# Performance work log

Hardware: AMD Instinct MI355X
Metric: run time of the kernel (lower is better)

The kernel has to match this reference:

```python
import jax, jax.numpy as jnp
import numpy as np

HIDDEN = 2048
N_HEADS = 32
N_KV_HEADS = 8
HEAD_DIM = HIDDEN // N_HEADS  # 64
N_REP = N_HEADS // N_KV_HEADS  # 4
ROPE_THETA = 10000.0


def setup_inputs() -> dict:
    key = jax.random.key(0)
    ks = jax.random.split(key, 5)
    b, s = 2, 2048
    x = jax.random.normal(ks[0], (b, s, HIDDEN), dtype=jnp.float32)
    position_ids = jnp.arange(b * s, dtype=jnp.int32).reshape(b, s)
    sc = 1.0 / np.sqrt(HIDDEN)
    Wq = jax.random.normal(ks[1], (HIDDEN, HIDDEN), dtype=jnp.float32) * sc
    Wk = jax.random.normal(ks[2], (HIDDEN, N_KV_HEADS * HEAD_DIM), dtype=jnp.float32) * sc
    Wv = jax.random.normal(ks[3], (HIDDEN, N_KV_HEADS * HEAD_DIM), dtype=jnp.float32) * sc
    Wo = jax.random.normal(ks[4], (HIDDEN, HIDDEN), dtype=jnp.float32) * sc
    return {"input_ids": x, "Wq": Wq, "Wk": Wk, "Wv": Wv, "Wo": Wo,
            "position_ids": position_ids}


def _rope_cos_sin(position_ids, dtype):
    # inv_freq: [head_dim/2]
    inv_freq = 1.0 / (ROPE_THETA ** (jnp.arange(0, HEAD_DIM, 2, dtype=jnp.float32) / HEAD_DIM))
    freqs = position_ids.astype(jnp.float32)[..., None] * inv_freq  # [b, s, d/2]
    emb = jnp.concatenate([freqs, freqs], axis=-1)  # [b, s, d]
    return emb.astype(dtype), None  # placeholder, replaced below


def _rotate_half(x):
    x1, x2 = jnp.split(x, 2, axis=-1)
    return jnp.concatenate([-x2, x1], axis=-1)


def reference(input_ids, Wq, Wk, Wv, Wo, position_ids):
    b, s, _ = input_ids.shape
    q = (input_ids @ Wq).reshape(b, s, N_HEADS, HEAD_DIM).transpose(0, 2, 1, 3)      # [b,H,s,d]
    k = (input_ids @ Wk).reshape(b, s, N_KV_HEADS, HEAD_DIM).transpose(0, 2, 1, 3)   # [b,Hkv,s,d]
    v = (input_ids @ Wv).reshape(b, s, N_KV_HEADS, HEAD_DIM).transpose(0, 2, 1, 3)

    # RoPE
    inv_freq = 1.0 / (ROPE_THETA ** (jnp.arange(0, HEAD_DIM, 2, dtype=jnp.float32) / HEAD_DIM))
    freqs = position_ids.astype(jnp.float32)[..., None] * inv_freq  # [b,s,d/2]
    emb = jnp.concatenate([freqs, freqs], axis=-1)                   # [b,s,d]
    cos = jnp.cos(emb).astype(input_ids.dtype)[:, None, :, :]        # [b,1,s,d]
    sin = jnp.sin(emb).astype(input_ids.dtype)[:, None, :, :]
    q = q * cos + _rotate_half(q) * sin
    k = k * cos + _rotate_half(k) * sin

    # repeat_kv: [b,Hkv,s,d] -> [b,H,s,d]
    k = jnp.repeat(k, N_REP, axis=1)
    v = jnp.repeat(v, N_REP, axis=1)

    # causal SDPA
    scale = 1.0 / np.sqrt(HEAD_DIM)
    scores = jnp.einsum('bhqd,bhkd->bhqk', q, k) * scale
    causal = jnp.tril(jnp.ones((s, s), dtype=bool))
    scores = jnp.where(causal, scores, jnp.finfo(scores.dtype).min)
    attn = jax.nn.softmax(scores, axis=-1)
    out = jnp.einsum('bhqk,bhkd->bhqd', attn, v)                     # [b,H,s,d]
    out = out.transpose(0, 2, 1, 3).reshape(b, s, HIDDEN)
    return out @ Wo
```

## Files before the change

kernel.cpp:

```cpp
#include <hip/hip_runtime.h>
#include <hip/hip_bf16.h>

#define HIDDEN 2048
#define NHEADS 32
#define NKVH   8
#define HD     64
#define BATCH  2
#define SEQ    2048
#define ROWS   (BATCH * SEQ)
#define NQKV   3072
#define KCOL   2048
#define VCOL   2560

typedef __bf16 bf16x8 __attribute__((ext_vector_type(8)));
typedef __bf16 bf16x4 __attribute__((ext_vector_type(4)));
typedef float  f32x4  __attribute__((ext_vector_type(4)));
typedef short  s16x4  __attribute__((ext_vector_type(4)));
typedef short  s16x8  __attribute__((ext_vector_type(8)));

__device__ __forceinline__ void gl2lds16(const void* g, void* l) {
  __builtin_amdgcn_global_load_lds(
      (const __attribute__((address_space(1))) void*)g,
      (__attribute__((address_space(3))) void*)l, 16, 0, 0);
}

__device__ __forceinline__ short f2bs(float f) {
  __bf16 h = (__bf16)f;
  return __builtin_bit_cast(short, h);
}

__device__ __forceinline__ float fexp2(float x) {
#if __has_builtin(__builtin_amdgcn_exp2f)
  return __builtin_amdgcn_exp2f(x);
#else
  return exp2f(x);
#endif
}

__device__ __forceinline__ f32x4 mfma16(s16x4 a, s16x4 b, f32x4 c) {
#if __has_builtin(__builtin_amdgcn_mfma_f32_16x16x16bf16_1k)
  return __builtin_amdgcn_mfma_f32_16x16x16bf16_1k(a, b, c, 0, 0, 0);
#else
  s16x8 a8 = __builtin_shufflevector(a, (s16x4){0,0,0,0}, 0,1,2,3,4,5,6,7);
  s16x8 b8 = __builtin_shufflevector(b, (s16x4){0,0,0,0}, 0,1,2,3,4,5,6,7);
  a8[4]=0;a8[5]=0;a8[6]=0;a8[7]=0; b8[4]=0;b8[5]=0;b8[6]=0;b8[7]=0;
  return __builtin_amdgcn_mfma_f32_16x16x32_bf16(
      __builtin_bit_cast(bf16x8, a8), __builtin_bit_cast(bf16x8, b8), c, 0, 0, 0);
#endif
}

__global__ void prep(const float* __restrict__ Wq, const float* __restrict__ Wk,
                     const float* __restrict__ Wv, const float* __restrict__ Wo,
                     const float* __restrict__ x,
                     __bf16* __restrict__ dstW, __bf16* __restrict__ Xb) {
  int bid = blockIdx.x, t = threadIdx.x;
  if (bid < 2560) {
    __shared__ __bf16 tl[32][132];
    int k0 = (bid & 15) * 128;
    int n0 = (bid >> 4) * 32;
    const float* src;
    int N, c0;
    if (n0 < 2048)      { src = Wq; N = 2048; c0 = n0; }
    else if (n0 < 2560) { src = Wk; N = 512;  c0 = n0 - 2048; }
    else if (n0 < 3072) { src = Wv; N = 512;  c0 = n0 - 2560; }
    else                { src = Wo; N = 2048; c0 = n0 - 3072; }
    int rr = t >> 3;
    int cc = (t & 7) * 4;
#pragma unroll
    for (int pass = 0; pass < 4; ++pass) {
      int k = pass * 32 + rr;
      float4 v = *(const float4*)(src + (size_t)(k0 + k) * N + c0 + cc);
      tl[cc + 0][k] = (__bf16)v.x;
      tl[cc + 1][k] = (__bf16)v.y;
      tl[cc + 2][k] = (__bf16)v.z;
      tl[cc + 3][k] = (__bf16)v.w;
    }
    __syncthreads();
    int n = t >> 4;
    int ch = t & 15;
#pragma unroll
    for (int it = 0; it < 2; ++it) {
      int nn = n + it * 16;
      s16x4 lo = *(const s16x4*)(&tl[nn][ch * 8]);
      s16x4 hi = *(const s16x4*)(&tl[nn][ch * 8 + 4]);
      s16x8 o = __builtin_shufflevector(lo, hi, 0, 1, 2, 3, 4, 5, 6, 7);
      *(s16x8*)(dstW + (size_t)(n0 + nn) * HIDDEN + k0 + ch * 8) = o;
    }
  } else {
    size_t i = (size_t)(bid - 2560) * 256 + t;
    const float4* s = (const float4*)(x + i * 16);
    float4 a = s[0], b = s[1], c = s[2], d = s[3];
    bf16x8 o0, o1;
    o0[0] = (__bf16)a.x; o0[1] = (__bf16)a.y; o0[2] = (__bf16)a.z; o0[3] = (__bf16)a.w;
    o0[4] = (__bf16)b.x; o0[5] = (__bf16)b.y; o0[6] = (__bf16)b.z; o0[7] = (__bf16)b.w;
    o1[0] = (__bf16)c.x; o1[1] = (__bf16)c.y; o1[2] = (__bf16)c.z; o1[3] = (__bf16)c.w;
    o1[4] = (__bf16)d.x; o1[5] = (__bf16)d.y; o1[6] = (__bf16)d.z; o1[7] = (__bf16)d.w;
    *(bf16x8*)(Xb + i * 16)     = o0;
    *(bf16x8*)(Xb + i * 16 + 8) = o1;
  }
}

template <typename OutT, bool ROPE>
__launch_bounds__(256, 2)
__global__ void gemm_bt(const __bf16* __restrict__ A, const __bf16* __restrict__ Bt,
                        OutT* __restrict__ C, int M, int N, int K,
                        const int* __restrict__ pos_ids, __bf16* __restrict__ Vt) {
  __shared__ __bf16 As[2][128 * 32];
  __shared__ __bf16 Bs[2][128 * 32];
  int id = blockIdx.x;
  int bm = (id & 7) * 4 + ((id >> 3) & 3);
  int bn = id >> 5;
  int t = threadIdx.x;
  int wave = t >> 6, lane = t & 63, l16 = lane & 15, quad = lane >> 4;
  int wm = (wave >> 1) * 64, wn = (wave & 1) * 64;

  f32x4 acc[4][4] = {};

  int arow = t >> 2;
  int ac   = (t & 3) * 8;
  const __bf16* Ag = A  + (size_t)(bm * 128 + arow) * K + ac;
  const __bf16* Bg = Bt + (size_t)(bn * 128 + arow) * K + ac;
  int woff = wave * 512;

  for (int k0 = 0; k0 < K; k0 += 64) {
    __syncthreads();
    gl2lds16(Ag + k0,                      &As[0][woff]);
    gl2lds16(Ag + (size_t)64 * K + k0,      &As[0][2048 + woff]);
    gl2lds16(Ag + k0 + 32,                 &As[1][woff]);
    gl2lds16(Ag + (size_t)64 * K + k0 + 32, &As[1][2048 + woff]);
    gl2lds16(Bg + k0,                      &Bs[0][woff]);
    gl2lds16(Bg + (size_t)64 * K + k0,      &Bs[0][2048 + woff]);
    gl2lds16(Bg + k0 + 32,                 &Bs[1][woff]);
    gl2lds16(Bg + (size_t)64 * K + k0 + 32, &Bs[1][2048 + woff]);
    __syncthreads();

#pragma unroll
    for (int ks = 0; ks < 2; ++ks) {
      bf16x8 af[4], bfr[4];
#pragma unroll
      for (int i = 0; i < 4; ++i) {
        af[i]  = *(const bf16x8*)(&As[ks][(wm + i * 16 + l16) * 32 + quad * 8]);
        bfr[i] = *(const bf16x8*)(&Bs[ks][(wn + i * 16 + l16) * 32 + quad * 8]);
      }
#pragma unroll
      for (int i = 0; i < 4; ++i)
#pragma unroll
        for (int j = 0; j < 4; ++j)
          acc[i][j] = __builtin_amdgcn_mfma_f32_16x16x32_bf16(af[i], bfr[j], acc[i][j], 0, 0, 0);
    }
  }

  if (ROPE) {
    int headidx = bn * 2 + (wn >> 6);
    if (headidx >= 40) {
#pragma unroll
      for (int i = 0; i < 4; ++i) {
        int srow = bm * 128 + wm + i * 16 + quad * 4;
        int b = srow >> 11, s = srow & 2047;
#pragma unroll
        for (int j = 0; j < 4; ++j) {
          int vcol = bn * 128 + wn + j * 16 + l16 - VCOL;
          int hk = vcol >> 6, d = vcol & 63;
          bf16x4 w;
#pragma unroll
          for (int r = 0; r < 4; ++r) w[r] = (__bf16)acc[i][j][r];
          *(bf16x4*)(Vt + ((size_t)(b * NKVH + hk) * HD + d) * SEQ + s) = w;
        }
      }
      return;
    }
    float invrev0 = __expf(-(float)l16 * 0.28782313662425574f) * 0.15915494309189535f;
    float invrev1 = __expf(-(float)(l16 + 16) * 0.28782313662425574f) * 0.15915494309189535f;
#pragma unroll
    for (int i = 0; i < 4; ++i)
#pragma unroll
      for (int r = 0; r < 4; ++r) {
        int gr = bm * 128 + wm + i * 16 + quad * 4 + r;
        float pos = (float)pos_ids[gr];
        float rv0 = pos * invrev0; rv0 -= floorf(rv0);
        float rv1 = pos * invrev1; rv1 -= floorf(rv1);
        float a0 = rv0 * 6.283185307179586f, a1 = rv1 * 6.283185307179586f;
        float s0 = __sinf(a0), c0 = __cosf(a0);
        float s1 = __sinf(a1), c1 = __cosf(a1);
        float x0 = acc[i][0][r], x2 = acc[i][2][r];
        acc[i][0][r] = x0 * c0 - x2 * s0;
        acc[i][2][r] = x2 * c0 + x0 * s0;
        float x1 = acc[i][1][r], x3 = acc[i][3][r];
        acc[i][1][r] = x1 * c1 - x3 * s1;
        acc[i][3][r] = x3 * c1 + x1 * s1;
      }
  }

#pragma unroll
  for (int i = 0; i < 4; ++i)
#pragma unroll
    for (int j = 0; j < 4; ++j)
#pragma unroll
      for (int r = 0; r < 4; ++r)
        C[(size_t)(bm * 128 + wm + i * 16 + quad * 4 + r) * N +
          (bn * 128 + wn + j * 16 + l16)] = (OutT)acc[i][j][r];
}

__launch_bounds__(256, 4)
__global__ void flash_attn(const __bf16* __restrict__ QKV, const __bf16* __restrict__ Vt,
                           __bf16* __restrict__ O) {
  int wgid = blockIdx.x + 64 * (blockIdx.y + 8 * (int)blockIdx.z);
  int xcd  = wgid & 7;
  int j    = wgid >> 3;
  int G    = j >> 6;
  int gid  = xcd * 2 + G;
  int b    = gid >> 3;
  int hk   = gid & 7;
  int r    = j & 63;
  int b0   = r & 1, b5 = (r >> 5) & 1;
  int h    = hk * 4 + b0 + 2 * b5;
  int M0   = (r >> 1) & 15;
  int M    = (b0 ^ b5) ? (15 - M0) : M0;
  int NT   = 2 * M + 2;

  int t = threadIdx.x;
  int wave = t >> 6, lane = t & 63, l16 = lane & 15, quad = lane >> 4;

  __shared__ __bf16 Ks[2][2][64 * 32];
  __shared__ __bf16 Vs[2][4096];

  const __bf16* Kbase = QKV + (size_t)(b * SEQ) * NQKV + KCOL + hk * HD;
  const __bf16* VtB   = Vt + (size_t)(b * NKVH + hk) * HD * SEQ;

  int kr  = wave * 16 + (lane >> 2);
  int kcs = ((lane & 3) ^ ((lane >> 3) & 3)) * 8;
  int rq  = (quad ^ ((l16 >> 1) & 3)) * 8;

  int vd   = kr;
  int vsc  = (lane & 3) * 16;
  int vs4w = (lane & 3) * 4;
  int vcw4 = (vd ^ (4 * (lane & 3))) * 4;

  const s16x4 vones = { (short)0x3F80, (short)0x3F80, (short)0x3F80, (short)0x3F80 };

  bf16x8 qfrag[2][2];
#pragma unroll
  for (int qi = 0; qi < 2; ++qi) {
    const __bf16* qp = QKV + (size_t)(b * SEQ + M * 128 + qi * 64 + wave * 16 + l16) * NQKV
                     + h * HD + quad * 8;
    bf16x8 q0 = *(const bf16x8*)qp;
    bf16x8 q1 = *(const bf16x8*)(qp + 32);
#pragma unroll
    for (int e = 0; e < 8; ++e) {
      qfrag[qi][0][e] = (__bf16)((float)q0[e] * 0.18033688011112042f);
      qfrag[qi][1][e] = (__bf16)((float)q1[e] * 0.18033688011112042f);
    }
  }

  f32x4 lacc[2] = { {0.f,0.f,0.f,0.f}, {0.f,0.f,0.f,0.f} };
  f32x4 oacc[2][4];
#pragma unroll
  for (int qi = 0; qi < 2; ++qi)
#pragma unroll
    for (int dt = 0; dt < 4; ++dt) oacc[qi][dt] = (f32x4){0.f, 0.f, 0.f, 0.f};

  {
    const __bf16* kp = Kbase + (size_t)kr * NQKV + kcs;
    gl2lds16(kp,      &Ks[0][0][wave * 512]);
    gl2lds16(kp + 32, &Ks[0][1][wave * 512]);
    const __bf16* vp = VtB + (size_t)vd * SEQ + vsc;
    s16x8 v0 = __builtin_bit_cast(s16x8, *(const bf16x8*)vp);
    s16x8 v1 = __builtin_bit_cast(s16x8, *(const bf16x8*)(vp + 8));
    *(s16x4*)(&Vs[0][(vs4w + 0) * 256 + vcw4]) = __builtin_shufflevector(v0, v0, 0, 1, 2, 3);
    *(s16x4*)(&Vs[0][(vs4w + 1) * 256 + vcw4]) = __builtin_shufflevector(v0, v0, 4, 5, 6, 7);
    *(s16x4*)(&Vs[0][(vs4w + 2) * 256 + vcw4]) = __builtin_shufflevector(v1, v1, 0, 1, 2, 3);
    *(s16x4*)(&Vs[0][(vs4w + 3) * 256 + vcw4]) = __builtin_shufflevector(v1, v1, 4, 5, 6, 7);
  }

  for (int kt = 0; kt < NT; ++kt) {
    int buf = kt & 1;
    __syncthreads();

    bool pre = (kt < NT - 1);
    s16x8 pv0, pv1;
    if (pre) {
      const __bf16* kp = Kbase + (size_t)((kt + 1) * 64 + kr) * NQKV + kcs;
      gl2lds16(kp,      &Ks[buf ^ 1][0][wave * 512]);
      gl2lds16(kp + 32, &Ks[buf ^ 1][1][wave * 512]);
      const __bf16* vp = VtB + (size_t)vd * SEQ + (kt + 1) * 64 + vsc;
      pv0 = __builtin_bit_cast(s16x8, *(const bf16x8*)vp);
      pv1 = __builtin_bit_cast(s16x8, *(const bf16x8*)(vp + 8));
    }

    f32x4 s0[4], s1[4];
#pragma unroll
    for (int nt = 0; nt < 4; ++nt) {
      s0[nt] = (f32x4){0.f, 0.f, 0.f, 0.f};
      s1[nt] = (f32x4){0.f, 0.f, 0.f, 0.f};
    }
#pragma unroll
    for (int ks = 0; ks < 2; ++ks) {
      bf16x8 kf[4];
#pragma unroll
      for (int nt = 0; nt < 4; ++nt)
        kf[nt] = *(const bf16x8*)(&Ks[buf][ks][(nt * 16 + l16) * 32 + rq]);
#pragma unroll
      for (int nt = 0; nt < 4; ++nt)
        s1[nt] = __builtin_amdgcn_mfma_f32_16x16x32_bf16(kf[nt], qfrag[1][ks], s1[nt], 0, 0, 0);
      if (pre) {
#pragma unroll
        for (int nt = 0; nt < 4; ++nt)
          s0[nt] = __builtin_amdgcn_mfma_f32_16x16x32_bf16(kf[nt], qfrag[0][ks], s0[nt], 0, 0, 0);
      }
    }

    s16x4 af0[4], af1[4];
    {
      int qg = wave * 16 + l16;
      if (kt == NT - 1) {
#pragma unroll
        for (int nt = 0; nt < 4; ++nt)
#pragma unroll
          for (int rr = 0; rr < 4; ++rr) {
            int kg = nt * 16 + quad * 4 + rr;
            af1[nt][rr] = f2bs(fexp2((kg > qg) ? -1e30f : s1[nt][rr]));
          }
      } else {
#pragma unroll
        for (int nt = 0; nt < 4; ++nt)
#pragma unroll
          for (int rr = 0; rr < 4; ++rr)
            af1[nt][rr] = f2bs(fexp2(s1[nt][rr]));
      }
      if (pre) {
        if (kt == NT - 2) {
#pragma unroll
          for (int nt = 0; nt < 4; ++nt)
#pragma unroll
            for (int rr = 0; rr < 4; ++rr) {
              int kg = nt * 16 + quad * 4 + rr;
              af0[nt][rr] = f2bs(fexp2((kg > qg) ? -1e30f : s0[nt][rr]));
            }
        } else {
#pragma unroll
          for (int nt = 0; nt < 4; ++nt)
#pragma unroll
            for (int rr = 0; rr < 4; ++rr)
              af0[nt][rr] = f2bs(fexp2(s0[nt][rr]));
        }
      }
    }

#pragma unroll
    for (int nt = 0; nt < 4; ++nt) {
      s16x4 vf[4];
#pragma unroll
      for (int dt = 0; dt < 4; ++dt)
        vf[dt] = *(const s16x4*)(&Vs[buf][(nt * 4 + quad) * 256 +
                                          (((dt * 16 + l16) ^ (nt * 4)) * 4)]);
#pragma unroll
      for (int dt = 0; dt < 4; ++dt)
        oacc[1][dt] = mfma16(af1[nt], vf[dt], oacc[1][dt]);
      lacc[1] = mfma16(af1[nt], vones, lacc[1]);
      if (pre) {
#pragma unroll
        for (int dt = 0; dt < 4; ++dt)
          oacc[0][dt] = mfma16(af0[nt], vf[dt], oacc[0][dt]);
        lacc[0] = mfma16(af0[nt], vones, lacc[0]);
      }
    }

    if (pre) {
      *(s16x4*)(&Vs[buf ^ 1][(vs4w + 0) * 256 + vcw4]) = __builtin_shufflevector(pv0, pv0, 0, 1, 2, 3);
      *(s16x4*)(&Vs[buf ^ 1][(vs4w + 1) * 256 + vcw4]) = __builtin_shufflevector(pv0, pv0, 4, 5, 6, 7);
      *(s16x4*)(&Vs[buf ^ 1][(vs4w + 2) * 256 + vcw4]) = __builtin_shufflevector(pv1, pv1, 0, 1, 2, 3);
      *(s16x4*)(&Vs[buf ^ 1][(vs4w + 3) * 256 + vcw4]) = __builtin_shufflevector(pv1, pv1, 4, 5, 6, 7);
    }
  }

#pragma unroll
  for (int qi = 0; qi < 2; ++qi) {
#pragma unroll
    for (int rr = 0; rr < 4; ++rr) {
      float inv = 1.0f / lacc[qi][rr];
#pragma unroll
      for (int dt = 0; dt < 4; ++dt) {
        float o = oacc[qi][dt][rr] * inv;
        O[(size_t)(b * SEQ + M * 128 + qi * 64 + wave * 16 + quad * 4 + rr) * HIDDEN +
          h * HD + dt * 16 + l16] = (__bf16)o;
      }
    }
  }
}

extern "C" void kernel_launch(void* const* d_in, const int* in_sizes, int n_in,
                              void* d_out, int out_size, void* d_ws, size_t ws_size,
                              hipStream_t stream) {
  const float* x  = (const float*)d_in[0];
  const float* Wq = (const float*)d_in[1];
  const float* Wk = (const float*)d_in[2];
  const float* Wv = (const float*)d_in[3];
  const float* Wo = (const float*)d_in[4];
  const int* pos  = (const int*)d_in[5];

  __bf16* Wqkvt = (__bf16*)d_ws;
  __bf16* Wot   = Wqkvt + (size_t)NQKV * HIDDEN;
  __bf16* Xb    = Wot + (size_t)HIDDEN * HIDDEN;
  __bf16* QKV   = Xb + (size_t)ROWS * HIDDEN;
  __bf16* Oat   = QKV + (size_t)ROWS * NQKV;
  __bf16* Vt    = Xb;

  prep<<<dim3(4608), 256, 0, stream>>>(Wq, Wk, Wv, Wo, x, Wqkvt, Xb);

  gemm_bt<__bf16, true><<<dim3(768), 256, 0, stream>>>(
      Xb, Wqkvt, QKV, ROWS, NQKV, HIDDEN, pos, Vt);

  flash_attn<<<dim3(64, NKVH, BATCH), 256, 0, stream>>>(QKV, Vt, Oat);

  gemm_bt<float, false><<<dim3(512), 256, 0, stream>>>(
      Oat, Wot, (float*)d_out, ROWS, HIDDEN, HIDDEN, nullptr, nullptr);
}
```

Measured before the change: 266.3 us.

## Replace QKV projection GEMM with 256x256-tile swizzled kernel and separate Vt buffer

Adds a dedicated QKV GEMM kernel that uses 256x256 output tiles, 512 threads, a 64-wide K step and XOR-swizzled LDS staging, with the RoPE and V-transpose epilogue carried over. Each block maps to an XCD-aware (bm, bn) pair. The goal is more reuse per LDS load and fewer bank conflicts than the generic 128x128 kernel. The trade-off is that only 192 blocks are launched, each using about 128KB of LDS and heavy accumulator registers, so some CUs may sit idle. Vt now goes to a dedicated workspace region when space allows, instead of aliasing the X buffer that the GEMM is still reading.

```diff
diff --git a/kernel.cpp b/kernel.cpp
--- a/kernel.cpp
+++ b/kernel.cpp
@@ -100,11 +100,123 @@
   }
 }
 
-template <typename OutT, bool ROPE>
+__launch_bounds__(512, 2)
+__global__ void gemm_qkv256(const __bf16* __restrict__ A, const __bf16* __restrict__ Bt,
+                            __bf16* __restrict__ C,
+                            const int* __restrict__ pos_ids, __bf16* __restrict__ Vt) {
+  __shared__ __bf16 As[2][16384];
+  __shared__ __bf16 Bs[2][16384];
+
+  int id = blockIdx.x;
+  int xcd = id & 7, j = id >> 3;
+  int bm = xcd * 2 + (j >= 12 ? 1 : 0);
+  int bn = (j >= 12) ? (j - 12) : j;
+
+  int t = threadIdx.x;
+  int wave = t >> 6, lane = t & 63, l16 = lane & 15, quad = lane >> 4;
+  int wml = (wave & 1) * 128;
+  int wnl = (wave >> 1) * 64;
+
+  int srow = wave * 8 + (lane >> 3);
+  int csrc = ((lane & 7) ^ (lane >> 3)) * 8;
+  const __bf16* Ag = A  + (size_t)(bm * 256 + srow) * HIDDEN + csrc;
+  const __bf16* Bg = Bt + (size_t)(bn * 256 + srow) * HIDDEN + csrc;
+
+  f32x4 acc[8][4] = {};
+
+#pragma unroll
+  for (int jj = 0; jj < 4; ++jj) {
+    gl2lds16(Ag + (size_t)jj * 64 * HIDDEN, &As[0][(jj * 64 + wave * 8) * 64]);
+    gl2lds16(Bg + (size_t)jj * 64 * HIDDEN, &Bs[0][(jj * 64 + wave * 8) * 64]);
+  }
+
+  for (int kt = 0; kt < 32; ++kt) {
+    int s = kt & 1;
+    __syncthreads();
+    if (kt < 31) {
+      const __bf16* Agk = Ag + (kt + 1) * 64;
+      const __bf16* Bgk = Bg + (kt + 1) * 64;
+#pragma unroll
+      for (int jj = 0; jj < 4; ++jj) {
+        gl2lds16(Agk + (size_t)jj * 64 * HIDDEN, &As[s ^ 1][(jj * 64 + wave * 8) * 64]);
+        gl2lds16(Bgk + (size_t)jj * 64 * HIDDEN, &Bs[s ^ 1][(jj * 64 + wave * 8) * 64]);
+      }
+    }
+#pragma unroll
+    for (int ks = 0; ks < 2; ++ks) {
+      int ch8 = (((ks * 4 + quad) ^ (l16 & 7))) * 8;
+      bf16x8 bfr[4];
+#pragma unroll
+      for (int n = 0; n < 4; ++n)
+        bfr[n] = *(const bf16x8*)(&Bs[s][(wnl + n * 16 + l16) * 64 + ch8]);
+#pragma unroll
+      for (int mh = 0; mh < 2; ++mh) {
+        bf16x8 af[4];
+#pragma unroll
+        for (int m = 0; m < 4; ++m)
+          af[m] = *(const bf16x8*)(&As[s][(wml + mh * 64 + m * 16 + l16) * 64 + ch8]);
+#pragma unroll
+        for (int m = 0; m < 4; ++m)
+#pragma unroll
+          for (int n = 0; n < 4; ++n)
+            acc[mh * 4 + m][n] =
+                __builtin_amdgcn_mfma_f32_16x16x32_bf16(af[m], bfr[n], acc[mh * 4 + m][n], 0, 0, 0);
+      }
+    }
+  }
+
+  int headidx = bn * 4 + (wave >> 1);
+  if (headidx >= 40) {
+    int hk = headidx - 40;
+#pragma unroll
+    for (int m = 0; m < 8; ++m) {
+      int gr0 = bm * 256 + wml + m * 16 + quad * 4;
+      int b = gr0 >> 11, sq = gr0 & 2047;
+#pragma unroll
+      for (int n = 0; n < 4; ++n) {
+        int d = n * 16 + l16;
+        bf16x4 w;
+#pragma unroll
+        for (int r = 0; r < 4; ++r) w[r] = (__bf16)acc[m][n][r];
+        *(bf16x4*)(Vt + ((size_t)(b * NKVH + hk) * HD + d) * SEQ + sq) = w;
+      }
+    }
+    return;
+  }
+  float invrev0 = __expf(-(float)l16 * 0.28782313662425574f) * 0.15915494309189535f;
+  float invrev1 = __expf(-(float)(l16 + 16) * 0.28782313662425574f) * 0.15915494309189535f;
+#pragma unroll
+  for (int m = 0; m < 8; ++m)
+#pragma unroll
+    for (int r = 0; r < 4; ++r) {
+      int gr = bm * 256 + wml + m * 16 + quad * 4 + r;
+      float pos = (float)pos_ids[gr];
+      float rv0 = pos * invrev0; rv0 -= floorf(rv0);
+      float rv1 = pos * invrev1; rv1 -= floorf(rv1);
+      float a0 = rv0 * 6.283185307179586f, a1 = rv1 * 6.283185307179586f;
+      float s0 = __sinf(a0), c0 = __cosf(a0);
+      float s1 = __sinf(a1), c1 = __cosf(a1);
+      float x0 = acc[m][0][r], x2 = acc[m][2][r];
+      acc[m][0][r] = x0 * c0 - x2 * s0;
+      acc[m][2][r] = x2 * c0 + x0 * s0;
+      float x1 = acc[m][1][r], x3 = acc[m][3][r];
+      acc[m][1][r] = x1 * c1 - x3 * s1;
+      acc[m][3][r] = x3 * c1 + x1 * s1;
+    }
+#pragma unroll
+  for (int m = 0; m < 8; ++m)
+#pragma unroll
+    for (int n = 0; n < 4; ++n)
+#pragma unroll
+      for (int r = 0; r < 4; ++r)
+        C[(size_t)(bm * 256 + wml + m * 16 + quad * 4 + r) * NQKV +
+          (bn * 256 + wnl + n * 16 + l16)] = (__bf16)acc[m][n][r];
+}
+
+template <typename OutT>
 __launch_bounds__(256, 2)
 __global__ void gemm_bt(const __bf16* __restrict__ A, const __bf16* __restrict__ Bt,
-                        OutT* __restrict__ C, int M, int N, int K,
-                        const int* __restrict__ pos_ids, __bf16* __restrict__ Vt) {
+                        OutT* __restrict__ C, int M, int N, int K) {
   __shared__ __bf16 As[2][128 * 32];
   __shared__ __bf16 Bs[2][128 * 32];
   int id = blockIdx.x;
@@ -148,47 +260,6 @@
         for (int j = 0; j < 4; ++j)
           acc[i][j] = __builtin_amdgcn_mfma_f32_16x16x32_bf16(af[i], bfr[j], acc[i][j], 0, 0, 0);
     }
-  }
-
-  if (ROPE) {
-    int headidx = bn * 2 + (wn >> 6);
-    if (headidx >= 40) {
-#pragma unroll
-      for (int i = 0; i < 4; ++i) {
-        int srow = bm * 128 + wm + i * 16 + quad * 4;
-        int b = srow >> 11, s = srow & 2047;
-#pragma unroll
-        for (int j = 0; j < 4; ++j) {
-          int vcol = bn * 128 + wn + j * 16 + l16 - VCOL;
-          int hk = vcol >> 6, d = vcol & 63;
-          bf16x4 w;
-#pragma unroll
-          for (int r = 0; r < 4; ++r) w[r] = (__bf16)acc[i][j][r];
-          *(bf16x4*)(Vt + ((size_t)(b * NKVH + hk) * HD + d) * SEQ + s) = w;
-        }
-      }
-      return;
-    }
-    float invrev0 = __expf(-(float)l16 * 0.28782313662425574f) * 0.15915494309189535f;
-    float invrev1 = __expf(-(float)(l16 + 16) * 0.28782313662425574f) * 0.15915494309189535f;
-#pragma unroll
-    for (int i = 0; i < 4; ++i)
-#pragma unroll
-      for (int r = 0; r < 4; ++r) {
-        int gr = bm * 128 + wm + i * 16 + quad * 4 + r;
-        float pos = (float)pos_ids[gr];
-        float rv0 = pos * invrev0; rv0 -= floorf(rv0);
-        float rv1 = pos * invrev1; rv1 -= floorf(rv1);
-        float a0 = rv0 * 6.283185307179586f, a1 = rv1 * 6.283185307179586f;
-        float s0 = __sinf(a0), c0 = __cosf(a0);
-        float s1 = __sinf(a1), c1 = __cosf(a1);
-        float x0 = acc[i][0][r], x2 = acc[i][2][r];
-        acc[i][0][r] = x0 * c0 - x2 * s0;
-        acc[i][2][r] = x2 * c0 + x0 * s0;
-        float x1 = acc[i][1][r], x3 = acc[i][3][r];
-        acc[i][1][r] = x1 * c1 - x3 * s1;
-        acc[i][3][r] = x3 * c1 + x1 * s1;
-      }
   }
 
 #pragma unroll
@@ -403,15 +474,17 @@
   __bf16* Xb    = Wot + (size_t)HIDDEN * HIDDEN;
   __bf16* QKV   = Xb + (size_t)ROWS * HIDDEN;
   __bf16* Oat   = QKV + (size_t)ROWS * NQKV;
-  __bf16* Vt    = Xb;
+
+  size_t need = ((size_t)(NQKV + HIDDEN) * HIDDEN + 2 * (size_t)ROWS * HIDDEN +
+                 (size_t)ROWS * NQKV + (size_t)BATCH * NKVH * HD * SEQ) * sizeof(__bf16);
+  __bf16* Vt = (ws_size >= need) ? (Oat + (size_t)ROWS * HIDDEN) : Xb;
 
   prep<<<dim3(4608), 256, 0, stream>>>(Wq, Wk, Wv, Wo, x, Wqkvt, Xb);
 
-  gemm_bt<__bf16, true><<<dim3(768), 256, 0, stream>>>(
-      Xb, Wqkvt, QKV, ROWS, NQKV, HIDDEN, pos, Vt);
+  gemm_qkv256<<<dim3(192), 512, 0, stream>>>(Xb, Wqkvt, QKV, pos, Vt);
 
   flash_attn<<<dim3(64, NKVH, BATCH), 256, 0, stream>>>(QKV, Vt, Oat);
 
-  gemm_bt<float, false><<<dim3(512), 256, 0, stream>>>(
-      Oat, Wot, (float*)d_out, ROWS, HIDDEN, HIDDEN, nullptr, nullptr);
-}
+  gemm_bt<float><<<dim3(512), 256, 0, stream>>>(
+      Oat, Wot, (float*)d_out, ROWS, HIDDEN, HIDDEN);
+}
```

Result: slower. 282.3 us (+6.0%).
